# Kernel tuning notes

Measured on AMD Instinct MI355X. Metric: run time of the kernel, lower is better.

## Reference

```python
import jax, jax.numpy as jnp
import numpy as np
import math

T, B, D = 256, 32, 512
H, HD, ETA, R = 8, 64, 4, 4
FEAT = HD * ETA
EPS = 1e-6


def setup_inputs() -> dict:
    key = jax.random.key(0)
    ks = jax.random.split(key, 14)
    w = lambda k, shape: jax.random.normal(k, shape, dtype=jnp.float32) * 0.03
    return {
        'inputs': jax.random.normal(ks[0], (T, B, D), dtype=jnp.float32) * 0.1,
        'terminations': jax.random.randint(ks[1], (T, B), 0, 2).astype(jnp.int32),
        'tilde_k_prev': jnp.zeros((B, R, H, FEAT), jnp.float32),
        'tilde_v_prev': jnp.zeros((B, R, H, HD), jnp.float32),
        's_prev': jnp.zeros((B, H, FEAT), jnp.float32),
        'tick': jnp.zeros((B,), jnp.float32),
        'Wq': w(ks[2], (H * HD, D)), 'Wk': w(ks[3], (H * HD, D)), 'Wv': w(ks[4], (H * HD, D)),
        'Wb': w(ks[5], (H * HD, D)), 'Wg': w(ks[6], (H * HD, D)),
        'Wp1': w(ks[7], (H * ETA, D)), 'Wp2': w(ks[8], (H * ETA, D)), 'Wp3': w(ks[9], (H * ETA, D)),
        'Wo': w(ks[10], (D, H * HD)), 'bo': jnp.zeros((D,), jnp.float32),
    }


def _feature_map(x, p):
    # x: (T,B,H,HD), p: (T,B,H,ETA) -> relu outer product -> (T,B,H,ETA*HD)
    f = jax.nn.relu(x[..., None, :] * p[..., :, None])
    return f.reshape(*f.shape[:3], FEAT)


def _gamma_map(g, p):
    # g in (0,1): (T,B,H,HD); p3 gated by sigmoid so result stays in (0,1)
    f = g[..., None, :] * jax.nn.sigmoid(p)[..., :, None]
    return f.reshape(*f.shape[:3], FEAT)


def _discounted_sum(prev, x, d):
    # s_t = d_t * s_{t-1} + x_t ; returns all T states
    def step(carry, xd):
        xi, di = xd
        carry = di * carry + xi
        return carry, carry
    _, ys = jax.lax.scan(step, prev, (x, d))
    return ys


def reference(inputs, terminations, tilde_k_prev, tilde_v_prev, s_prev, tick,
              Wq, Wk, Wv, Wb, Wg, Wp1, Wp2, Wp3, Wo, bo):
    proj = lambda W, n: jnp.einsum('tbd,ed->tbe', inputs, W).reshape(T, B, H, n)
    q = proj(Wq, HD); k = proj(Wk, HD); v = proj(Wv, HD)
    beta = jax.nn.sigmoid(proj(Wb, HD))
    gamma = jax.nn.sigmoid(proj(Wg, HD))
    p1 = proj(Wp1, ETA); p2 = proj(Wp2, ETA); p3 = proj(Wp3, ETA)

    phi_q = _feature_map(q, p2)      # (T,B,H,FEAT)
    psi_k = _feature_map(k, p1)
    gamma_feat = _gamma_map(gamma, p3)

    omegas = jnp.linspace(-math.pi, math.pi, R).astype(jnp.float32)
    steps = jnp.arange(1, T + 1, dtype=jnp.float32)
    cos_step = jnp.cos(steps[:, None] * omegas)   # (T,R)
    sin_step = jnp.sin(steps[:, None] * omegas)
    ang_tick = tick[:, None] * omegas             # (B,R)
    cos_terms = (jnp.cos(ang_tick)[None] * cos_step[:, None]
                 - jnp.sin(ang_tick)[None] * sin_step[:, None])  # (T,B,R)

    gated_v = v * beta                      # (T,B,H,HD)
    gated_k = psi_k * gamma_feat            # (T,B,H,FEAT)
    ce = cos_terms[..., None, None]         # (T,B,R,1,1)
    values_osc = gated_v[:, :, None] * ce   # (T,B,R,H,HD)
    keys_osc = gated_k[:, :, None] * ce     # (T,B,R,H,FEAT)

    term_mask = (1.0 - terminations.astype(jnp.float32))[..., None, None]  # (T,B,1,1)
    disc_gamma = (1.0 - gamma_feat) * term_mask   # (T,B,H,FEAT)
    disc_beta = (1.0 - beta) * term_mask          # (T,B,H,HD)

    final_keys = _discounted_sum(tilde_k_prev, keys_osc, disc_gamma[:, :, None])
    final_values = _discounted_sum(tilde_v_prev, values_osc, disc_beta[:, :, None])
    final_s = _discounted_sum(s_prev, gated_k, disc_gamma)

    kdq = jnp.einsum('tbrhD,tbhD->tbrh', final_keys, phi_q)
    kv = jnp.einsum('tbrhd,tbrh->tbhd', final_values, kdq)
    norm = jnp.einsum('tbhD,tbhD->tbh', final_s, phi_q)
    attn = kv / (2.0 * R * norm[..., None] + EPS)
    out = jnp.einsum('tbe,de->tbd', attn.reshape(T, B, H * HD), Wo) + bo
    return out
```

## Files before the change

### kernel.cpp

```cpp
#include <hip/hip_runtime.h>
#include <hip/hip_bf16.h>

#define T_N 256
#define B_N 32
#define D_N 512
#define H_N 8
#define HD_N 64
#define ETA_N 4
#define R_N 4
#define FEAT_N 256
#define NCOL 2688
#define TB_N (T_N * B_N)
#define NCHUNK 32
#define CLEN 8

using bf16 = __hip_bfloat16;
typedef __attribute__((ext_vector_type(8))) short short8;
typedef __attribute__((ext_vector_type(4))) float f32x4;
typedef __attribute__((ext_vector_type(4))) unsigned short u16x4;

__device__ __forceinline__ float sigmoidf_(float x) { return 1.f / (1.f + __expf(-x)); }
__device__ __forceinline__ float b2f(unsigned short u) {
  union { unsigned int i; float f; } x; x.i = ((unsigned int)u) << 16; return x.f;
}

__global__ void cast_f32_to_bf16_vec4(const float* __restrict__ src,
                                      bf16* __restrict__ dst, int n4) {
  int i = blockIdx.x * blockDim.x + threadIdx.x;
  if (i < n4) {
    float4 v = reinterpret_cast<const float4*>(src)[i];
    bf16* d = dst + (size_t)i * 4;
    d[0] = __float2bfloat16(v.x);
    d[1] = __float2bfloat16(v.y);
    d[2] = __float2bfloat16(v.z);
    d[3] = __float2bfloat16(v.w);
  }
}

__global__ void build_wcat(const float* __restrict__ Wq, const float* __restrict__ Wk,
                           const float* __restrict__ Wv, const float* __restrict__ Wb,
                           const float* __restrict__ Wg, const float* __restrict__ Wp1,
                           const float* __restrict__ Wp2, const float* __restrict__ Wp3,
                           bf16* __restrict__ Wcat) {
  int i = blockIdx.x * blockDim.x + threadIdx.x;
  if (i >= NCOL * D_N) return;
  int r = i >> 9, k = i & 511;
  float v = 0.f;
  if      (r <  512) v = Wq [(r       ) * D_N + k];
  else if (r < 1024) v = Wk [(r -  512) * D_N + k];
  else if (r < 1536) v = Wv [(r - 1024) * D_N + k];
  else if (r < 2048) v = Wb [(r - 1536) * D_N + k];
  else if (r < 2560) v = Wg [(r - 2048) * D_N + k];
  else if (r < 2592) v = Wp1[(r - 2560) * D_N + k];
  else if (r < 2624) v = Wp2[(r - 2592) * D_N + k];
  else if (r < 2656) v = Wp3[(r - 2624) * D_N + k];
  Wcat[i] = __float2bfloat16(v);
}

template <typename OutT>
__global__ __launch_bounds__(256) void gemm_bt_bf16(
    const bf16* __restrict__ A, const bf16* __restrict__ Bm,
    OutT* __restrict__ C, const float* __restrict__ bias,
    int K, int ldc) {
  __shared__ __align__(16) bf16 As[128 * 32];
  __shared__ __align__(16) bf16 Bs[128 * 32];
  const int tid = threadIdx.x;
  const int w = tid >> 6, l = tid & 63;
  const size_t tm = (size_t)blockIdx.x * 128;
  const size_t tn = (size_t)blockIdx.y * 128;
  const int lr = l & 15, lk8 = (l >> 4) * 8;
  const int wr = (w >> 1) * 64, wc = (w & 1) * 64;
  f32x4 acc[4][4] = {};

  for (int kt = 0; kt < K; kt += 32) {
    __syncthreads();
#pragma unroll
    for (int j = 0; j < 2; ++j) {
      int q = (w * 2 + j) * 64 + l;
      int row = q >> 2, cc = (q & 3) * 8;
      __builtin_amdgcn_global_load_lds(
          (const __attribute__((address_space(1))) void*)(A + (tm + row) * K + kt + cc),
          (__attribute__((address_space(3))) void*)(As + q * 8), 16, 0, 0);
      __builtin_amdgcn_global_load_lds(
          (const __attribute__((address_space(1))) void*)(Bm + (tn + row) * K + kt + cc),
          (__attribute__((address_space(3))) void*)(Bs + q * 8), 16, 0, 0);
    }
    __syncthreads();
    short8 af[4], bfr[4];
#pragma unroll
    for (int i = 0; i < 4; ++i)
      af[i] = *reinterpret_cast<const short8*>(As + (wr + i * 16 + lr) * 32 + lk8);
#pragma unroll
    for (int i = 0; i < 4; ++i)
      bfr[i] = *reinterpret_cast<const short8*>(Bs + (wc + i * 16 + lr) * 32 + lk8);
#pragma unroll
    for (int i = 0; i < 4; ++i)
#pragma unroll
      for (int j = 0; j < 4; ++j)
        acc[i][j] = __builtin_amdgcn_mfma_f32_16x16x32_bf16(af[i], bfr[j], acc[i][j], 0, 0, 0);
  }

  const int oc = l & 15, orow = (l >> 4) * 4;
#pragma unroll
  for (int i = 0; i < 4; ++i)
#pragma unroll
    for (int j = 0; j < 4; ++j) {
      size_t col = tn + wc + j * 16 + oc;
      float bv = bias ? bias[col] : 0.f;
#pragma unroll
      for (int v = 0; v < 4; ++v) {
        size_t row = tm + wr + i * 16 + orow + v;
        float val = acc[i][j][v] + bv;
        if constexpr (__is_same(OutT, bf16))
          C[row * ldc + col] = __float2bfloat16(val);
        else
          C[row * ldc + col] = val;
      }
    }
}

__global__ __launch_bounds__(64) void scan_pass1(
    const unsigned short* __restrict__ proj, const int* __restrict__ term,
    const float* __restrict__ tick, float* __restrict__ Pa, bf16* __restrict__ Ea) {
  const int bc = blockIdx.x;
  const int bh = bc >> 5, c = bc & (NCHUNK - 1);
  const int b = bh >> 3, h = bh & 7;
  const int lane = threadIdx.x;
  const int t0 = c * CLEN;
  const int koff = 512 + h * HD_N + lane;

  unsigned short kv8[CLEN], vv8[CLEN], bl8[CLEN], gl8[CLEN];
  u16x4 p18[CLEN], p38[CLEN];
  int tm8[CLEN];
#pragma unroll
  for (int tt = 0; tt < CLEN; ++tt) {
    const unsigned short* rw = proj + (size_t)((t0 + tt) * B_N + b) * NCOL;
    kv8[tt] = rw[koff];
    vv8[tt] = rw[512 + koff];
    bl8[tt] = rw[1024 + koff];
    gl8[tt] = rw[1536 + koff];
    p18[tt] = *(const u16x4*)(rw + 2560 + h * 4);
    p38[tt] = *(const u16x4*)(rw + 2624 + h * 4);
    tm8[tt] = term[(t0 + tt) * B_N + b];
  }

  float s_st[ETA_N] = {};
  float k_st[ETA_N][R_N] = {};
  float v_st[R_N] = {};
  float Pg[ETA_N] = {1.f, 1.f, 1.f, 1.f};
  float Pb = 1.f;

  float ce[R_N], se[R_N], cw[R_N], sw[R_N];
  const float tk = tick[b];
#pragma unroll
  for (int r = 0; r < R_N; ++r) {
    float w = -3.14159265358979323846f + 2.09439510239319549231f * (float)r;
    float a0 = (tk + (float)(t0 + 1)) * w;
    ce[r] = cosf(a0); se[r] = sinf(a0);
    cw[r] = cosf(w);  sw[r] = sinf(w);
  }

#pragma unroll
  for (int tt = 0; tt < CLEN; ++tt) {
    float k = b2f(kv8[tt]), v = b2f(vv8[tt]);
    float mask  = 1.f - (float)tm8[tt];
    float gamma = sigmoidf_(b2f(gl8[tt]));
    float beta  = sigmoidf_(b2f(bl8[tt]));
    float p1a[4]  = {b2f(p18[tt][0]), b2f(p18[tt][1]), b2f(p18[tt][2]), b2f(p18[tt][3])};
    float sp3a[4] = {sigmoidf_(b2f(p38[tt][0])), sigmoidf_(b2f(p38[tt][1])),
                     sigmoidf_(b2f(p38[tt][2])), sigmoidf_(b2f(p38[tt][3]))};

#pragma unroll
    for (int e = 0; e < ETA_N; ++e) {
      float psi = fmaxf(k * p1a[e], 0.f);
      float gf  = gamma * sp3a[e];
      float gk  = psi * gf;
      float dg  = (1.f - gf) * mask;
      s_st[e] = dg * s_st[e] + gk;
      Pg[e] *= dg;
#pragma unroll
      for (int r = 0; r < R_N; ++r)
        k_st[e][r] = dg * k_st[e][r] + gk * ce[r];
    }
    float gv = v * beta;
    float db = (1.f - beta) * mask;
    Pb *= db;
#pragma unroll
    for (int r = 0; r < R_N; ++r)
      v_st[r] = db * v_st[r] + gv * ce[r];

#pragma unroll
    for (int r = 0; r < R_N; ++r) {
      float c2 = ce[r] * cw[r] - se[r] * sw[r];
      float s2 = se[r] * cw[r] + ce[r] * sw[r];
      ce[r] = c2; se[r] = s2;
    }
  }

  float* pa = Pa + (size_t)(bh * NCHUNK + c) * 320;
#pragma unroll
  for (int e = 0; e < ETA_N; ++e) pa[e * 64 + lane] = Pg[e];
  pa[256 + lane] = Pb;
  bf16* ea = Ea + (size_t)(bh * NCHUNK + c) * 1536;
#pragma unroll
  for (int e = 0; e < ETA_N; ++e) ea[e * 64 + lane] = __float2bfloat16(s_st[e]);
#pragma unroll
  for (int e = 0; e < ETA_N; ++e)
#pragma unroll
    for (int r = 0; r < R_N; ++r)
      ea[256 + (e * 4 + r) * 64 + lane] = __float2bfloat16(k_st[e][r]);
#pragma unroll
  for (int r = 0; r < R_N; ++r) ea[1280 + r * 64 + lane] = __float2bfloat16(v_st[r]);
}

__global__ __launch_bounds__(256) void scan_pass2(
    const float* __restrict__ Pa, bf16* __restrict__ Ea,
    const float* __restrict__ tkp, const float* __restrict__ tvp,
    const float* __restrict__ sp) {
  const int elem = blockIdx.x * 256 + threadIdx.x;
  const int bh = blockIdx.y;
  const int b = bh >> 3, h = bh & 7;
  int poff; float cr;
  if (elem < 256) {
    cr = sp[(b * H_N + h) * FEAT_N + elem];
    poff = elem;
  } else if (elem < 1280) {
    int el = elem - 256;
    int e = el >> 8, r = (el >> 6) & 3, d = el & 63;
    cr = tkp[((b * R_N + r) * H_N + h) * FEAT_N + e * 64 + d];
    poff = e * 64 + d;
  } else {
    int el = elem - 1280;
    int r = el >> 6, d = el & 63;
    cr = tvp[((b * R_N + r) * H_N + h) * HD_N + d];
    poff = 256 + d;
  }
  size_t ip = (size_t)(bh * NCHUNK) * 320 + poff;
  size_t ie = (size_t)(bh * NCHUNK) * 1536 + elem;
  float p = Pa[ip];
  float e = __bfloat162float(Ea[ie]);
  for (int c = 0; c < NCHUNK; ++c) {
    float pn = 0.f, en = 0.f;
    if (c + 1 < NCHUNK) { pn = Pa[ip + 320]; en = __bfloat162float(Ea[ie + 1536]); }
    Ea[ie] = __float2bfloat16(cr);
    cr = p * cr + e;
    p = pn; e = en; ip += 320; ie += 1536;
  }
}

__global__ __launch_bounds__(64) void scan_pass3(
    const unsigned short* __restrict__ proj, const int* __restrict__ term,
    const bf16* __restrict__ Ea, const float* __restrict__ tick,
    bf16* __restrict__ attn) {
  const int bc = blockIdx.x;
  const int bh = bc >> 5, c = bc & (NCHUNK - 1);
  const int b = bh >> 3, h = bh & 7;
  const int lane = threadIdx.x;
  const int t0 = c * CLEN;
  const int qoff = h * HD_N + lane;

  unsigned short qv8[CLEN], kv8[CLEN], vv8[CLEN], bl8[CLEN], gl8[CLEN];
  u16x4 p18[CLEN], p28[CLEN], p38[CLEN];
  int tm8[CLEN];
#pragma unroll
  for (int tt = 0; tt < CLEN; ++tt) {
    const unsigned short* rw = proj + (size_t)((t0 + tt) * B_N + b) * NCOL;
    qv8[tt] = rw[qoff];
    kv8[tt] = rw[512 + qoff];
    vv8[tt] = rw[1024 + qoff];
    bl8[tt] = rw[1536 + qoff];
    gl8[tt] = rw[2048 + qoff];
    p18[tt] = *(const u16x4*)(rw + 2560 + h * 4);
    p28[tt] = *(const u16x4*)(rw + 2592 + h * 4);
    p38[tt] = *(const u16x4*)(rw + 2624 + h * 4);
    tm8[tt] = term[(t0 + tt) * B_N + b];
  }

  const bf16* cb = Ea + (size_t)(bh * NCHUNK + c) * 1536;
  float s_st[ETA_N], k_st[ETA_N][R_N], v_st[R_N];
#pragma unroll
  for (int e = 0; e < ETA_N; ++e) s_st[e] = __bfloat162float(cb[e * 64 + lane]);
#pragma unroll
  for (int e = 0; e < ETA_N; ++e)
#pragma unroll
    for (int r = 0; r < R_N; ++r)
      k_st[e][r] = __bfloat162float(cb[256 + (e * 4 + r) * 64 + lane]);
#pragma unroll
  for (int r = 0; r < R_N; ++r) v_st[r] = __bfloat162float(cb[1280 + r * 64 + lane]);

  float ce[R_N], se[R_N], cw[R_N], sw[R_N];
  const float tk = tick[b];
#pragma unroll
  for (int r = 0; r < R_N; ++r) {
    float w = -3.14159265358979323846f + 2.09439510239319549231f * (float)r;
    float a0 = (tk + (float)(t0 + 1)) * w;
    ce[r] = cosf(a0); se[r] = sinf(a0);
    cw[r] = cosf(w);  sw[r] = sinf(w);
  }

#pragma unroll
  for (int tt = 0; tt < CLEN; ++tt) {
    float q = b2f(qv8[tt]), k = b2f(kv8[tt]), v = b2f(vv8[tt]);
    float mask  = 1.f - (float)tm8[tt];
    float gamma = sigmoidf_(b2f(gl8[tt]));
    float beta  = sigmoidf_(b2f(bl8[tt]));
    float p1a[4]  = {b2f(p18[tt][0]), b2f(p18[tt][1]), b2f(p18[tt][2]), b2f(p18[tt][3])};
    float p2a[4]  = {b2f(p28[tt][0]), b2f(p28[tt][1]), b2f(p28[tt][2]), b2f(p28[tt][3])};
    float sp3a[4] = {sigmoidf_(b2f(p38[tt][0])), sigmoidf_(b2f(p38[tt][1])),
                     sigmoidf_(b2f(p38[tt][2])), sigmoidf_(b2f(p38[tt][3]))};

    float norm_p = 0.f, kdq0 = 0.f, kdq1 = 0.f, kdq2 = 0.f, kdq3 = 0.f;
#pragma unroll
    for (int e = 0; e < ETA_N; ++e) {
      float psi = fmaxf(k * p1a[e], 0.f);
      float gf  = gamma * sp3a[e];
      float gk  = psi * gf;
      float dg  = (1.f - gf) * mask;
      float phi = fmaxf(q * p2a[e], 0.f);
      s_st[e] = dg * s_st[e] + gk;
      norm_p += s_st[e] * phi;
      k_st[e][0] = dg * k_st[e][0] + gk * ce[0]; kdq0 += k_st[e][0] * phi;
      k_st[e][1] = dg * k_st[e][1] + gk * ce[1]; kdq1 += k_st[e][1] * phi;
      k_st[e][2] = dg * k_st[e][2] + gk * ce[2]; kdq2 += k_st[e][2] * phi;
      k_st[e][3] = dg * k_st[e][3] + gk * ce[3]; kdq3 += k_st[e][3] * phi;
    }
#pragma unroll
    for (int m = 1; m < 64; m <<= 1) {
      norm_p += __shfl_xor(norm_p, m);
      kdq0 += __shfl_xor(kdq0, m);
      kdq1 += __shfl_xor(kdq1, m);
      kdq2 += __shfl_xor(kdq2, m);
      kdq3 += __shfl_xor(kdq3, m);
    }
    float gv = v * beta;
    float db = (1.f - beta) * mask;
    v_st[0] = db * v_st[0] + gv * ce[0];
    v_st[1] = db * v_st[1] + gv * ce[1];
    v_st[2] = db * v_st[2] + gv * ce[2];
    v_st[3] = db * v_st[3] + gv * ce[3];
    float kv = v_st[0] * kdq0 + v_st[1] * kdq1 + v_st[2] * kdq2 + v_st[3] * kdq3;
    float a = kv / (8.f * norm_p + 1e-6f);
    attn[((size_t)((t0 + tt) * B_N + b) * H_N + h) * HD_N + lane] = __float2bfloat16(a);
#pragma unroll
    for (int r = 0; r < R_N; ++r) {
      float c2 = ce[r] * cw[r] - se[r] * sw[r];
      float s2 = se[r] * cw[r] + ce[r] * sw[r];
      ce[r] = c2; se[r] = s2;
    }
  }
}

extern "C" void kernel_launch(void* const* d_in, const int* in_sizes, int n_in,
                              void* d_out, int out_size, void* d_ws, size_t ws_size,
                              hipStream_t stream) {
  const float* x    = (const float*)d_in[0];
  const int*   term = (const int*)  d_in[1];
  const float* tkp  = (const float*)d_in[2];
  const float* tvp  = (const float*)d_in[3];
  const float* sp   = (const float*)d_in[4];
  const float* tick = (const float*)d_in[5];
  const float* Wq   = (const float*)d_in[6];
  const float* Wk   = (const float*)d_in[7];
  const float* Wv   = (const float*)d_in[8];
  const float* Wb   = (const float*)d_in[9];
  const float* Wg   = (const float*)d_in[10];
  const float* Wp1  = (const float*)d_in[11];
  const float* Wp2  = (const float*)d_in[12];
  const float* Wp3  = (const float*)d_in[13];
  const float* Wo   = (const float*)d_in[14];
  const float* bo   = (const float*)d_in[15];
  float* out = (float*)d_out;

  char* ws = (char*)d_ws;
  bf16*  projb = (bf16*) (ws);
  bf16*  Xb    = (bf16*) (ws + 44040192);
  bf16*  Wcat  = (bf16*) (ws + 52428800);
  bf16*  Wob   = (bf16*) (ws + 55181312);
  bf16*  Ea    = (bf16*) (ws + 55705600);
  float* Pa    = (float*)(ws + 80871424);
  bf16*  attn  = (bf16*) (ws + 91357184);

  cast_f32_to_bf16_vec4<<<4096, 256, 0, stream>>>(x, Xb, TB_N * D_N / 4);
  cast_f32_to_bf16_vec4<<<256, 256, 0, stream>>>(Wo, Wob, D_N * D_N / 4);
  build_wcat<<<(NCOL * D_N + 255) / 256, 256, 0, stream>>>(Wq, Wk, Wv, Wb, Wg, Wp1, Wp2, Wp3, Wcat);

  gemm_bt_bf16<bf16><<<dim3(TB_N / 128, NCOL / 128), 256, 0, stream>>>(
      Xb, Wcat, projb, nullptr, D_N, NCOL);

  const unsigned short* proju = (const unsigned short*)projb;
  scan_pass1<<<B_N * H_N * NCHUNK, 64, 0, stream>>>(proju, term, tick, Pa, Ea);
  scan_pass2<<<dim3(6, 256), 256, 0, stream>>>(Pa, Ea, tkp, tvp, sp);
  scan_pass3<<<B_N * H_N * NCHUNK, 64, 0, stream>>>(proju, term, Ea, tick, attn);

  gemm_bt_bf16<float><<<dim3(TB_N / 128, D_N / 128), 256, 0, stream>>>(
      attn, Wob, out, bo, D_N, D_N);
}
```

Before: 229.6 us.

## Double-buffer LDS tiles and XOR-swizzle chunks in bf16 GEMM

The bf16 MFMA GEMM now keeps two LDS buffers for the A and B tiles. It issues the global-to-LDS load for the next K tile before doing the MFMAs on the current one, so the loads overlap with compute and one barrier per iteration is dropped. The 16-byte chunks within each LDS row are also XOR-swizzled by row index, on both the write and read sides, to cut bank conflicts on the short8 fragment reads. This doubles the LDS footprint per block, which may reduce occupancy.

```diff
diff --git a/kernel.cpp b/kernel.cpp
--- a/kernel.cpp
+++ b/kernel.cpp
@@ -62,42 +62,56 @@
     const bf16* __restrict__ A, const bf16* __restrict__ Bm,
     OutT* __restrict__ C, const float* __restrict__ bias,
     int K, int ldc) {
-  __shared__ __align__(16) bf16 As[128 * 32];
-  __shared__ __align__(16) bf16 Bs[128 * 32];
+  __shared__ __align__(16) bf16 As[2][128 * 32];
+  __shared__ __align__(16) bf16 Bs[2][128 * 32];
   const int tid = threadIdx.x;
   const int w = tid >> 6, l = tid & 63;
   const size_t tm = (size_t)blockIdx.x * 128;
   const size_t tn = (size_t)blockIdx.y * 128;
-  const int lr = l & 15, lk8 = (l >> 4) * 8;
+  const int lr = l & 15, lchunk = l >> 4;
   const int wr = (w >> 1) * 64, wc = (w & 1) * 64;
   f32x4 acc[4][4] = {};
 
-  for (int kt = 0; kt < K; kt += 32) {
-    __syncthreads();
+  auto stage = [&](int buf, int kt) {
 #pragma unroll
     for (int j = 0; j < 2; ++j) {
       int q = (w * 2 + j) * 64 + l;
-      int row = q >> 2, cc = (q & 3) * 8;
+      int row = q >> 2, cs = q & 3;
+      int src = cs ^ ((row >> 1) & 3);
       __builtin_amdgcn_global_load_lds(
-          (const __attribute__((address_space(1))) void*)(A + (tm + row) * K + kt + cc),
-          (__attribute__((address_space(3))) void*)(As + q * 8), 16, 0, 0);
+          (const __attribute__((address_space(1))) void*)(A + (tm + row) * K + kt + src * 8),
+          (__attribute__((address_space(3))) void*)(&As[buf][q * 8]), 16, 0, 0);
       __builtin_amdgcn_global_load_lds(
-          (const __attribute__((address_space(1))) void*)(Bm + (tn + row) * K + kt + cc),
-          (__attribute__((address_space(3))) void*)(Bs + q * 8), 16, 0, 0);
-    }
+          (const __attribute__((address_space(1))) void*)(Bm + (tn + row) * K + kt + src * 8),
+          (__attribute__((address_space(3))) void*)(&Bs[buf][q * 8]), 16, 0, 0);
+    }
+  };
+
+  stage(0, 0);
+  int cur = 0;
+  const int NT = K / 32;
+  for (int t = 0; t < NT; ++t) {
     __syncthreads();
+    if (t + 1 < NT) stage(cur ^ 1, (t + 1) * 32);
     short8 af[4], bfr[4];
 #pragma unroll
-    for (int i = 0; i < 4; ++i)
-      af[i] = *reinterpret_cast<const short8*>(As + (wr + i * 16 + lr) * 32 + lk8);
-#pragma unroll
-    for (int i = 0; i < 4; ++i)
-      bfr[i] = *reinterpret_cast<const short8*>(Bs + (wc + i * 16 + lr) * 32 + lk8);
+    for (int i = 0; i < 4; ++i) {
+      int row = wr + i * 16 + lr;
+      int cs = lchunk ^ ((row >> 1) & 3);
+      af[i] = *reinterpret_cast<const short8*>(&As[cur][row * 32 + cs * 8]);
+    }
+#pragma unroll
+    for (int i = 0; i < 4; ++i) {
+      int row = wc + i * 16 + lr;
+      int cs = lchunk ^ ((row >> 1) & 3);
+      bfr[i] = *reinterpret_cast<const short8*>(&Bs[cur][row * 32 + cs * 8]);
+    }
 #pragma unroll
     for (int i = 0; i < 4; ++i)
 #pragma unroll
       for (int j = 0; j < 4; ++j)
         acc[i][j] = __builtin_amdgcn_mfma_f32_16x16x32_bf16(af[i], bfr[j], acc[i][j], 0, 0, 0);
+    cur ^= 1;
   }
 
   const int oc = l & 15, orow = (l >> 4) * 4;
```

Result: no change. 227.2 us (-1.1%).
